# Optimization experiments

Hardware: AMD Instinct MI355X
Metric: run time of the kernel (lower is better)

The kernel has to match this reference:

```python
import jax, jax.numpy as jnp
import numpy as np

INPUT_DIM = 1024
CODEBOOK_DIM = 128
CODEBOOK_SIZE = 8192
B, N = 8, 4096


def setup_inputs() -> dict:
    key = jax.random.key(0)
    k1, k2, k3 = jax.random.split(key, 3)
    x = jax.random.normal(k1, (B, N, INPUT_DIM), dtype=jnp.float32)
    # xavier_normal_: std = sqrt(2 / (fan_in + fan_out))
    xavier_std = float(np.sqrt(2.0 / (INPUT_DIM + CODEBOOK_DIM)))
    random_projection = jax.random.normal(k2, (INPUT_DIM, CODEBOOK_DIM), dtype=jnp.float32) * xavier_std
    codebook = jax.random.normal(k3, (CODEBOOK_SIZE, CODEBOOK_DIM), dtype=jnp.float32)
    return {"x": x, "random_projection": random_projection, "codebook": codebook}


def reference(x, random_projection, codebook):
    # random projection: [B, N, D] @ [D, E] -> [B, N, E]
    proj = jnp.einsum("bnd,de->bne", x, random_projection)
    b, n, e = proj.shape
    flat = proj.reshape(b * n, e)  # [BN, E]
    eps = 1e-12  # matches torch F.normalize default eps
    nx = flat / jnp.maximum(jnp.linalg.norm(flat, axis=1, keepdims=True), eps)
    ncb = codebook / jnp.maximum(jnp.linalg.norm(codebook, axis=1, keepdims=True), eps)
    # squared euclidean distances [K, BN]; argmin of d^2 == argmin of cdist
    d2 = (
        jnp.sum(ncb * ncb, axis=1)[:, None]
        + jnp.sum(nx * nx, axis=1)[None, :]
        - 2.0 * (ncb @ nx.T)
    )
    nearest = jnp.argmin(d2, axis=0)  # [BN]
    return nearest.reshape(b, n).astype(jnp.int32)
```

## Files before the change

kernel.cpp:

```cpp
#include <hip/hip_runtime.h>
#include <math.h>
#include <float.h>
#include <limits.h>

#define BN      32768
#define D_IN    1024
#define E_DIM   128
#define CB_N    8192

typedef _Float16 f16x8 __attribute__((ext_vector_type(8)));
typedef _Float16 f16x4 __attribute__((ext_vector_type(4)));
typedef float    f32x4 __attribute__((ext_vector_type(4)));


__global__ __launch_bounds__(256) void pack_kernel(
    const float* __restrict__ cb, const float* __restrict__ rp,
    _Float16* __restrict__ ph, _Float16* __restrict__ pl,
    _Float16* __restrict__ rph, _Float16* __restrict__ rpl) {
    const int t = threadIdx.x;
    if (blockIdx.x < 512) {
        __shared__ float L[16][129];
        const int g = blockIdx.x;
        const int c = t >> 4, p = t & 15;
        const float4 v0 = *(const float4*)&cb[(size_t)(g * 16 + c) * E_DIM + p * 8];
        const float4 v1 = *(const float4*)&cb[(size_t)(g * 16 + c) * E_DIM + p * 8 + 4];
        float ss = v0.x * v0.x + v0.y * v0.y + v0.z * v0.z + v0.w * v0.w
                 + v1.x * v1.x + v1.y * v1.y + v1.z * v1.z + v1.w * v1.w;
#pragma unroll
        for (int m = 1; m < 16; m <<= 1) ss += __shfl_xor(ss, m);
        const float inv = 256.0f / fmaxf(sqrtf(ss), 1e-12f);

        L[c][p * 8 + 0] = v0.x * inv; L[c][p * 8 + 1] = v0.y * inv;
        L[c][p * 8 + 2] = v0.z * inv; L[c][p * 8 + 3] = v0.w * inv;
        L[c][p * 8 + 4] = v1.x * inv; L[c][p * 8 + 5] = v1.y * inv;
        L[c][p * 8 + 6] = v1.z * inv; L[c][p * 8 + 7] = v1.w * inv;
        __syncthreads();

        const int kb = t >> 6, lane = t & 63;
        const int quad = (lane >> 4), col = lane & 15;
        f16x8 h, l;
#pragma unroll
        for (int j = 0; j < 8; ++j) {
            const float v = L[col][kb * 32 + quad * 8 + j];
            const _Float16 hv = (_Float16)v;
            h[j] = hv;
            l[j] = (_Float16)(v - (float)hv);
        }
        const size_t off = ((size_t)(g * 4 + kb) * 64 + lane) * 8;
        *(f16x8*)&ph[off] = h;
        *(f16x8*)&pl[off] = l;
    } else {
        const int w = t >> 6, lane = t & 63;
        const int b = (blockIdx.x - 512) * 4 + w;
        const int kb = b >> 3, nt = b & 7;
        const int quad = lane >> 4, col = lane & 15;
        f16x8 h, l;
#pragma unroll
        for (int j = 0; j < 8; ++j) {
            const float v = rp[(size_t)(kb * 32 + quad * 8 + j) * E_DIM + nt * 16 + col] * 64.0f;
            const _Float16 hv = (_Float16)v;
            h[j] = hv;
            l[j] = (_Float16)(v - (float)hv);
        }
        const size_t off = ((size_t)b * 64 + lane) * 8;
        *(f16x8*)&rph[off] = h;
        *(f16x8*)&rpl[off] = l;
    }
}

#define PAD_ROW 40
#define PPITCH  132

__global__ __launch_bounds__(256, 2) void fused_kernel(
    const float* __restrict__ x,
    const _Float16* __restrict__ rph, const _Float16* __restrict__ rpl,
    const _Float16* __restrict__ ph, const _Float16* __restrict__ pl,
    int* __restrict__ out) {
    __shared__ _Float16 Ah[64 * PAD_ROW];
    __shared__ _Float16 Al[64 * PAD_ROW];
    __shared__ float    P[64 * PPITCH];
    __shared__ float    ls[4][32];
    __shared__ int      li[4][32];

    const int tid  = threadIdx.x;
    const int lane = tid & 63;
    const int w    = tid >> 6;
    const int quad = lane >> 4, col = lane & 15;
    const int qb   = blockIdx.x * 64;

    const int srow = tid >> 3;
    const int skc  = (tid & 7) * 4;

    f32x4 acc[4][2];
#pragma unroll
    for (int mt = 0; mt < 4; ++mt)
#pragma unroll
        for (int h = 0; h < 2; ++h) acc[mt][h] = (f32x4){0.f, 0.f, 0.f, 0.f};

    float4 pre[2];
#pragma unroll
    for (int i = 0; i < 2; ++i)
        pre[i] = *(const float4*)&x[(size_t)(qb + srow + 32 * i) * D_IN + skc];

    for (int kb = 0; kb < 32; ++kb) {
#pragma unroll
        for (int i = 0; i < 2; ++i) {
            const float vv[4] = {pre[i].x, pre[i].y, pre[i].z, pre[i].w};
            f16x4 h4, l4;
#pragma unroll
            for (int j = 0; j < 4; ++j) {
                const float v = vv[j] * 512.0f;
                const _Float16 hv = (_Float16)v;
                h4[j] = hv;
                l4[j] = (_Float16)(v - (float)hv);
            }
            const int base = (srow + 32 * i) * PAD_ROW + skc;
            *(f16x4*)&Ah[base] = h4;
            *(f16x4*)&Al[base] = l4;
        }
        __syncthreads();

        if (kb + 1 < 32) {
#pragma unroll
            for (int i = 0; i < 2; ++i)
                pre[i] = *(const float4*)&x[(size_t)(qb + srow + 32 * i) * D_IN + (kb + 1) * 32 + skc];
        }

        f16x8 bh1[2], bl1[2];
#pragma unroll
        for (int h = 0; h < 2; ++h) {
            const int nt = w * 2 + h;
            const size_t off = ((size_t)(kb * 8 + nt) * 64 + lane) * 8;
            bh1[h] = *(const f16x8*)&rph[off];
            bl1[h] = *(const f16x8*)&rpl[off];
        }

        f16x8 ah1[4], al1[4];
#pragma unroll
        for (int mt = 0; mt < 4; ++mt) {
            const int base = (mt * 16 + col) * PAD_ROW + quad * 8;
            ah1[mt] = *(const f16x8*)&Ah[base];
            al1[mt] = *(const f16x8*)&Al[base];
        }

#pragma unroll
        for (int mt = 0; mt < 4; ++mt)
#pragma unroll
            for (int h = 0; h < 2; ++h)
                acc[mt][h] = __builtin_amdgcn_mfma_f32_16x16x32_f16(ah1[mt], bh1[h], acc[mt][h], 0, 0, 0);
#pragma unroll
        for (int mt = 0; mt < 4; ++mt)
#pragma unroll
            for (int h = 0; h < 2; ++h)
                acc[mt][h] = __builtin_amdgcn_mfma_f32_16x16x32_f16(ah1[mt], bl1[h], acc[mt][h], 0, 0, 0);
#pragma unroll
        for (int mt = 0; mt < 4; ++mt)
#pragma unroll
            for (int h = 0; h < 2; ++h)
                acc[mt][h] = __builtin_amdgcn_mfma_f32_16x16x32_f16(al1[mt], bh1[h], acc[mt][h], 0, 0, 0);

        __syncthreads();
    }

#pragma unroll
    for (int mt = 0; mt < 4; ++mt)
#pragma unroll
        for (int h = 0; h < 2; ++h)
#pragma unroll
            for (int r = 0; r < 4; ++r) {
                const int row = mt * 16 + quad * 4 + r;
                const int cc  = w * 32 + h * 16 + col;
                P[row * PPITCH + cc] = acc[mt][h][r] * (1.0f / 2048.0f);
            }
    __syncthreads();

    const int wq = w >> 1;
    const int wc = w & 1;

    f16x8 ah[2][4], al[2][4];
#pragma unroll
    for (int mt2 = 0; mt2 < 2; ++mt2)
#pragma unroll
        for (int kb = 0; kb < 4; ++kb) {
            const int base = (wq * 32 + mt2 * 16 + col) * PPITCH + kb * 32 + quad * 8;
            const float4 v0 = *(const float4*)&P[base];
            const float4 v1 = *(const float4*)&P[base + 4];
            const float vv[8] = {v0.x, v0.y, v0.z, v0.w, v1.x, v1.y, v1.z, v1.w};
            f16x8 hh, ll;
#pragma unroll
            for (int j = 0; j < 8; ++j) {
                const _Float16 hv = (_Float16)vv[j];
                hh[j] = hv;
                ll[j] = (_Float16)(vv[j] - (float)hv);
            }
            ah[mt2][kb] = hh;
            al[mt2][kb] = ll;
        }

    float bs[8];
    int   bi[8];
#pragma unroll
    for (int s = 0; s < 8; ++s) { bs[s] = -FLT_MAX; bi[s] = 0; }

    const int g0 = wc * 256;

    f16x8 bh[2][4], bl[2][4];
#pragma unroll
    for (int kb = 0; kb < 4; ++kb) {
        const size_t off = ((size_t)(g0 * 4 + kb) * 64 + lane) * 8;
        bh[0][kb] = *(const f16x8*)&ph[off];
        bl[0][kb] = *(const f16x8*)&pl[off];
    }

#pragma unroll 2
    for (int t = 0; t < 256; ++t) {
        const int cur = t & 1, nxt = cur ^ 1;
        if (t + 1 < 256) {
            const int gn = g0 + t + 1;
#pragma unroll
            for (int kb = 0; kb < 4; ++kb) {
                const size_t off = ((size_t)(gn * 4 + kb) * 64 + lane) * 8;
                bh[nxt][kb] = *(const f16x8*)&ph[off];
                bl[nxt][kb] = *(const f16x8*)&pl[off];
            }
        }

        f32x4 a0h = (f32x4){0.f, 0.f, 0.f, 0.f}, a0m = a0h, a0l = a0h;
        f32x4 a1h = a0h, a1m = a0h, a1l = a0h;

#pragma unroll
        for (int kb = 0; kb < 4; ++kb) {
            a0h = __builtin_amdgcn_mfma_f32_16x16x32_f16(ah[0][kb], bh[cur][kb], a0h, 0, 0, 0);
            a1h = __builtin_amdgcn_mfma_f32_16x16x32_f16(ah[1][kb], bh[cur][kb], a1h, 0, 0, 0);
            a0m = __builtin_amdgcn_mfma_f32_16x16x32_f16(ah[0][kb], bl[cur][kb], a0m, 0, 0, 0);
            a1m = __builtin_amdgcn_mfma_f32_16x16x32_f16(ah[1][kb], bl[cur][kb], a1m, 0, 0, 0);
            a0l = __builtin_amdgcn_mfma_f32_16x16x32_f16(al[0][kb], bh[cur][kb], a0l, 0, 0, 0);
            a1l = __builtin_amdgcn_mfma_f32_16x16x32_f16(al[1][kb], bh[cur][kb], a1l, 0, 0, 0);
        }

        const f32x4 s0 = a0h + a0m + a0l;
        const f32x4 s1 = a1h + a1m + a1l;

        const int code = (g0 + t) * 16 + col;
#pragma unroll
        for (int r = 0; r < 4; ++r) {
            if (s0[r] > bs[r])     { bs[r] = s0[r];     bi[r] = code; }
            if (s1[r] > bs[4 + r]) { bs[4 + r] = s1[r]; bi[4 + r] = code; }
        }
    }

#pragma unroll
    for (int s = 0; s < 8; ++s) {
#pragma unroll
        for (int m = 1; m < 16; m <<= 1) {
            const float os = __shfl_xor(bs[s], m);
            const int   oi = __shfl_xor(bi[s], m);
            if (os > bs[s] || (os == bs[s] && oi < bi[s])) { bs[s] = os; bi[s] = oi; }
        }
    }

    if (col == 0) {
#pragma unroll
        for (int mt2 = 0; mt2 < 2; ++mt2)
#pragma unroll
            for (int r = 0; r < 4; ++r) {
                ls[w][mt2 * 16 + quad * 4 + r] = bs[mt2 * 4 + r];
                li[w][mt2 * 16 + quad * 4 + r] = bi[mt2 * 4 + r];
            }
    }
    __syncthreads();

    if (tid < 64) {
        const int q   = tid;
        const int wq2 = q >> 5;
        const int q32 = q & 31;
        float s = ls[wq2 * 2 + 0][q32];
        int   i = li[wq2 * 2 + 0][q32];
        const float os = ls[wq2 * 2 + 1][q32];
        if (os > s) { s = os; i = li[wq2 * 2 + 1][q32]; }
        out[qb + q] = i;
    }
}

extern "C" void kernel_launch(void* const* d_in, const int* in_sizes, int n_in,
                              void* d_out, int out_size, void* d_ws, size_t ws_size,
                              hipStream_t stream) {
    const float* x  = (const float*)d_in[0];
    const float* rp = (const float*)d_in[1];
    const float* cb = (const float*)d_in[2];
    int* out = (int*)d_out;

    _Float16* ph  = (_Float16*)d_ws;
    _Float16* pl  = ph  + (size_t)CB_N * E_DIM;
    _Float16* rph = pl  + (size_t)CB_N * E_DIM;
    _Float16* rpl = rph + (size_t)D_IN * E_DIM;

    pack_kernel<<<576, 256, 0, stream>>>(cb, rp, ph, pl, rph, rpl);
    fused_kernel<<<BN / 64, 256, 0, stream>>>(x, rph, rpl, ph, pl, out);
}
```

Measured before the change: 402.7 us.

## Switch codebook distance search to 32x32x16 MFMA with repacked codebook layout

The codebook search phase now uses 32x32x16 f16 MFMA tiles instead of 16x16x32: each wave handles 32 query rows against 32-code tiles, and the pack kernel lays out the split-f16 codebook in the matching 32-column, 16-deep fragment order. The larger tile doubles reuse per fragment load and cuts the number of MFMA instructions and argmax updates per code. In exchange the explicit double-buffered prefetch of codebook fragments is dropped in favour of per-iteration loads with no unrolling, and more accumulator and index registers are live, which may raise register pressure and expose load latency.

```diff
diff --git a/kernel.cpp b/kernel.cpp
--- a/kernel.cpp
+++ b/kernel.cpp
@@ -8,50 +8,60 @@
 #define E_DIM   128
 #define CB_N    8192
 
-typedef _Float16 f16x8 __attribute__((ext_vector_type(8)));
-typedef _Float16 f16x4 __attribute__((ext_vector_type(4)));
-typedef float    f32x4 __attribute__((ext_vector_type(4)));
+typedef _Float16 f16x8  __attribute__((ext_vector_type(8)));
+typedef _Float16 f16x4  __attribute__((ext_vector_type(4)));
+typedef float    f32x4  __attribute__((ext_vector_type(4)));
+typedef float    f32x16 __attribute__((ext_vector_type(16)));
 
 
 __global__ __launch_bounds__(256) void pack_kernel(
     const float* __restrict__ cb, const float* __restrict__ rp,
-    _Float16* __restrict__ ph, _Float16* __restrict__ pl,
+    _Float16* __restrict__ pb, _Float16* __restrict__ plb,
     _Float16* __restrict__ rph, _Float16* __restrict__ rpl) {
     const int t = threadIdx.x;
-    if (blockIdx.x < 512) {
-        __shared__ float L[16][129];
+    if (blockIdx.x < 256) {
+        __shared__ float L[32][130];
         const int g = blockIdx.x;
-        const int c = t >> 4, p = t & 15;
-        const float4 v0 = *(const float4*)&cb[(size_t)(g * 16 + c) * E_DIM + p * 8];
-        const float4 v1 = *(const float4*)&cb[(size_t)(g * 16 + c) * E_DIM + p * 8 + 4];
-        float ss = v0.x * v0.x + v0.y * v0.y + v0.z * v0.z + v0.w * v0.w
-                 + v1.x * v1.x + v1.y * v1.y + v1.z * v1.z + v1.w * v1.w;
-#pragma unroll
-        for (int m = 1; m < 16; m <<= 1) ss += __shfl_xor(ss, m);
+        const int c = t >> 3, p = t & 7;
+        float ss = 0.0f;
+        float4 v[4];
+#pragma unroll
+        for (int i = 0; i < 4; ++i) {
+            v[i] = *(const float4*)&cb[(size_t)(g * 32 + c) * E_DIM + p * 16 + i * 4];
+            ss += v[i].x * v[i].x + v[i].y * v[i].y + v[i].z * v[i].z + v[i].w * v[i].w;
+        }
+#pragma unroll
+        for (int m = 1; m < 8; m <<= 1) ss += __shfl_xor(ss, m);
         const float inv = 256.0f / fmaxf(sqrtf(ss), 1e-12f);
-
-        L[c][p * 8 + 0] = v0.x * inv; L[c][p * 8 + 1] = v0.y * inv;
-        L[c][p * 8 + 2] = v0.z * inv; L[c][p * 8 + 3] = v0.w * inv;
-        L[c][p * 8 + 4] = v1.x * inv; L[c][p * 8 + 5] = v1.y * inv;
-        L[c][p * 8 + 6] = v1.z * inv; L[c][p * 8 + 7] = v1.w * inv;
+#pragma unroll
+        for (int i = 0; i < 4; ++i) {
+            L[c][p * 16 + i * 4 + 0] = v[i].x * inv;
+            L[c][p * 16 + i * 4 + 1] = v[i].y * inv;
+            L[c][p * 16 + i * 4 + 2] = v[i].z * inv;
+            L[c][p * 16 + i * 4 + 3] = v[i].w * inv;
+        }
         __syncthreads();
 
-        const int kb = t >> 6, lane = t & 63;
-        const int quad = (lane >> 4), col = lane & 15;
-        f16x8 h, l;
-#pragma unroll
-        for (int j = 0; j < 8; ++j) {
-            const float v = L[col][kb * 32 + quad * 8 + j];
-            const _Float16 hv = (_Float16)v;
-            h[j] = hv;
-            l[j] = (_Float16)(v - (float)hv);
-        }
-        const size_t off = ((size_t)(g * 4 + kb) * 64 + lane) * 8;
-        *(f16x8*)&ph[off] = h;
-        *(f16x8*)&pl[off] = l;
+        const int lane = t & 63;
+        const int n32  = lane & 31, kh = lane >> 5;
+#pragma unroll
+        for (int ks2 = 0; ks2 < 2; ++ks2) {
+            const int ks = (t >> 6) * 2 + ks2;
+            f16x8 h, l;
+#pragma unroll
+            for (int j = 0; j < 8; ++j) {
+                const float vv = L[n32][ks * 16 + kh * 8 + j];
+                const _Float16 hv = (_Float16)vv;
+                h[j] = hv;
+                l[j] = (_Float16)(vv - (float)hv);
+            }
+            const size_t off = ((size_t)(g * 8 + ks) * 64 + lane) * 8;
+            *(f16x8*)&pb[off]  = h;
+            *(f16x8*)&plb[off] = l;
+        }
     } else {
         const int w = t >> 6, lane = t & 63;
-        const int b = (blockIdx.x - 512) * 4 + w;
+        const int b = (blockIdx.x - 256) * 4 + w;
         const int kb = b >> 3, nt = b & 7;
         const int quad = lane >> 4, col = lane & 15;
         f16x8 h, l;
@@ -74,7 +84,7 @@
 __global__ __launch_bounds__(256, 2) void fused_kernel(
     const float* __restrict__ x,
     const _Float16* __restrict__ rph, const _Float16* __restrict__ rpl,
-    const _Float16* __restrict__ ph, const _Float16* __restrict__ pl,
+    const _Float16* __restrict__ pb, const _Float16* __restrict__ plb,
     int* __restrict__ out) {
     __shared__ _Float16 Ah[64 * PAD_ROW];
     __shared__ _Float16 Al[64 * PAD_ROW];
@@ -174,110 +184,90 @@
             }
     __syncthreads();
 
-    const int wq = w >> 1;
-    const int wc = w & 1;
-
-    f16x8 ah[2][4], al[2][4];
-#pragma unroll
-    for (int mt2 = 0; mt2 < 2; ++mt2)
-#pragma unroll
-        for (int kb = 0; kb < 4; ++kb) {
-            const int base = (wq * 32 + mt2 * 16 + col) * PPITCH + kb * 32 + quad * 8;
-            const float4 v0 = *(const float4*)&P[base];
-            const float4 v1 = *(const float4*)&P[base + 4];
-            const float vv[8] = {v0.x, v0.y, v0.z, v0.w, v1.x, v1.y, v1.z, v1.w};
-            f16x8 hh, ll;
-#pragma unroll
-            for (int j = 0; j < 8; ++j) {
-                const _Float16 hv = (_Float16)vv[j];
-                hh[j] = hv;
-                ll[j] = (_Float16)(vv[j] - (float)hv);
-            }
-            ah[mt2][kb] = hh;
-            al[mt2][kb] = ll;
-        }
-
-    float bs[8];
-    int   bi[8];
-#pragma unroll
-    for (int s = 0; s < 8; ++s) { bs[s] = -FLT_MAX; bi[s] = 0; }
-
-    const int g0 = wc * 256;
-
-    f16x8 bh[2][4], bl[2][4];
-#pragma unroll
-    for (int kb = 0; kb < 4; ++kb) {
-        const size_t off = ((size_t)(g0 * 4 + kb) * 64 + lane) * 8;
-        bh[0][kb] = *(const f16x8*)&ph[off];
-        bl[0][kb] = *(const f16x8*)&pl[off];
-    }
-
-#pragma unroll 2
-    for (int t = 0; t < 256; ++t) {
-        const int cur = t & 1, nxt = cur ^ 1;
-        if (t + 1 < 256) {
-            const int gn = g0 + t + 1;
-#pragma unroll
-            for (int kb = 0; kb < 4; ++kb) {
-                const size_t off = ((size_t)(gn * 4 + kb) * 64 + lane) * 8;
-                bh[nxt][kb] = *(const f16x8*)&ph[off];
-                bl[nxt][kb] = *(const f16x8*)&pl[off];
-            }
-        }
-
-        f32x4 a0h = (f32x4){0.f, 0.f, 0.f, 0.f}, a0m = a0h, a0l = a0h;
-        f32x4 a1h = a0h, a1m = a0h, a1l = a0h;
-
-#pragma unroll
-        for (int kb = 0; kb < 4; ++kb) {
-            a0h = __builtin_amdgcn_mfma_f32_16x16x32_f16(ah[0][kb], bh[cur][kb], a0h, 0, 0, 0);
-            a1h = __builtin_amdgcn_mfma_f32_16x16x32_f16(ah[1][kb], bh[cur][kb], a1h, 0, 0, 0);
-            a0m = __builtin_amdgcn_mfma_f32_16x16x32_f16(ah[0][kb], bl[cur][kb], a0m, 0, 0, 0);
-            a1m = __builtin_amdgcn_mfma_f32_16x16x32_f16(ah[1][kb], bl[cur][kb], a1m, 0, 0, 0);
-            a0l = __builtin_amdgcn_mfma_f32_16x16x32_f16(al[0][kb], bh[cur][kb], a0l, 0, 0, 0);
-            a1l = __builtin_amdgcn_mfma_f32_16x16x32_f16(al[1][kb], bh[cur][kb], a1l, 0, 0, 0);
-        }
-
-        const f32x4 s0 = a0h + a0m + a0l;
-        const f32x4 s1 = a1h + a1m + a1l;
-
-        const int code = (g0 + t) * 16 + col;
-#pragma unroll
-        for (int r = 0; r < 4; ++r) {
-            if (s0[r] > bs[r])     { bs[r] = s0[r];     bi[r] = code; }
-            if (s1[r] > bs[4 + r]) { bs[4 + r] = s1[r]; bi[4 + r] = code; }
-        }
-    }
-
-#pragma unroll
-    for (int s = 0; s < 8; ++s) {
-#pragma unroll
-        for (int m = 1; m < 16; m <<= 1) {
+    const int wq  = w >> 1;
+    const int wc  = w & 1;
+    const int n32 = lane & 31, kh = lane >> 5;
+
+    f16x8 ah[8], al[8];
+#pragma unroll
+    for (int ks = 0; ks < 8; ++ks) {
+        const int base = (wq * 32 + n32) * PPITCH + ks * 16 + kh * 8;
+        const float4 v0 = *(const float4*)&P[base];
+        const float4 v1 = *(const float4*)&P[base + 4];
+        const float vv[8] = {v0.x, v0.y, v0.z, v0.w, v1.x, v1.y, v1.z, v1.w};
+        f16x8 hh, ll;
+#pragma unroll
+        for (int j = 0; j < 8; ++j) {
+            const _Float16 hv = (_Float16)vv[j];
+            hh[j] = hv;
+            ll[j] = (_Float16)(vv[j] - (float)hv);
+        }
+        ah[ks] = hh;
+        al[ks] = ll;
+    }
+
+    float bs[16];
+    int   bi[16];
+#pragma unroll
+    for (int s = 0; s < 16; ++s) { bs[s] = -FLT_MAX; bi[s] = 0; }
+
+    const int g0 = wc * 128;
+
+#pragma unroll 1
+    for (int t = 0; t < 128; ++t) {
+        const int g = g0 + t;
+        f16x8 bh[8], bl[8];
+#pragma unroll
+        for (int ks = 0; ks < 8; ++ks) {
+            const size_t off = ((size_t)(g * 8 + ks) * 64 + lane) * 8;
+            bh[ks] = *(const f16x8*)&pb[off];
+            bl[ks] = *(const f16x8*)&plb[off];
+        }
+
+        f32x16 am = (f32x16)(0.0f), c1 = (f32x16)(0.0f), c2 = (f32x16)(0.0f);
+#pragma unroll
+        for (int ks = 0; ks < 8; ++ks) {
+            am = __builtin_amdgcn_mfma_f32_32x32x16_f16(ah[ks], bh[ks], am, 0, 0, 0);
+            c1 = __builtin_amdgcn_mfma_f32_32x32x16_f16(ah[ks], bl[ks], c1, 0, 0, 0);
+            c2 = __builtin_amdgcn_mfma_f32_32x32x16_f16(al[ks], bh[ks], c2, 0, 0, 0);
+        }
+        const f32x16 s = am + c1 + c2;
+
+        const int code = g * 32 + n32;
+#pragma unroll
+        for (int r = 0; r < 16; ++r) {
+            if (s[r] > bs[r]) { bs[r] = s[r]; bi[r] = code; }
+        }
+    }
+
+#pragma unroll
+    for (int s = 0; s < 16; ++s) {
+#pragma unroll
+        for (int m = 1; m < 32; m <<= 1) {
             const float os = __shfl_xor(bs[s], m);
             const int   oi = __shfl_xor(bi[s], m);
             if (os > bs[s] || (os == bs[s] && oi < bi[s])) { bs[s] = os; bi[s] = oi; }
         }
     }
 
-    if (col == 0) {
-#pragma unroll
-        for (int mt2 = 0; mt2 < 2; ++mt2)
-#pragma unroll
-            for (int r = 0; r < 4; ++r) {
-                ls[w][mt2 * 16 + quad * 4 + r] = bs[mt2 * 4 + r];
-                li[w][mt2 * 16 + quad * 4 + r] = bi[mt2 * 4 + r];
-            }
+    if (n32 == 0) {
+#pragma unroll
+        for (int r = 0; r < 16; ++r) {
+            const int row = (r & 3) + 8 * (r >> 2) + 4 * kh;
+            ls[w][row] = bs[r];
+            li[w][row] = bi[r];
+        }
     }
     __syncthreads();
 
     if (tid < 64) {
-        const int q   = tid;
-        const int wq2 = q >> 5;
-        const int q32 = q & 31;
-        float s = ls[wq2 * 2 + 0][q32];
-        int   i = li[wq2 * 2 + 0][q32];
-        const float os = ls[wq2 * 2 + 1][q32];
-        if (os > s) { s = os; i = li[wq2 * 2 + 1][q32]; }
+        const int q     = tid;
+        const int qtile = q >> 5;
+        const int row   = q & 31;
+        float s = ls[qtile * 2 + 0][row];
+        int   i = li[qtile * 2 + 0][row];
+        const float os = ls[qtile * 2 + 1][row];
+        if (os > s) { s = os; i = li[qtile * 2 + 1][row]; }
         out[qb + q] = i;
     }
 }
@@ -290,11 +280,11 @@
     const float* cb = (const float*)d_in[2];
     int* out = (int*)d_out;
 
-    _Float16* ph  = (_Float16*)d_ws;
-    _Float16* pl  = ph  + (size_t)CB_N * E_DIM;
-    _Float16* rph = pl  + (size_t)CB_N * E_DIM;
+    _Float16* pb  = (_Float16*)d_ws;
+    _Float16* plb = pb  + (size_t)CB_N * E_DIM;
+    _Float16* rph = plb + (size_t)CB_N * E_DIM;
     _Float16* rpl = rph + (size_t)D_IN * E_DIM;
 
-    pack_kernel<<<576, 256, 0, stream>>>(cb, rp, ph, pl, rph, rpl);
-    fused_kernel<<<BN / 64, 256, 0, stream>>>(x, rph, rpl, ph, pl, out);
+    pack_kernel<<<320, 256, 0, stream>>>(cb, rp, pb, plb, rph, rpl);
+    fused_kernel<<<BN / 64, 256, 0, stream>>>(x, rph, rpl, pb, plb, out);
 }
```

Measured after the change: 708.7 us. 1.76x slower.
